# Performance work log

Hardware: AMD Instinct MI355X
Metric: run time of the kernel (lower is better)

The kernel has to match this reference:

```python
import jax, jax.numpy as jnp
import numpy as np

B, S, H = 4, 8192, 1024


def setup_inputs() -> dict:
    key = jax.random.key(0)
    kq, kk, kv, k1, k2, k3, k4 = jax.random.split(key, 7)
    residual_init_factor = 1.0
    return {
        "q": jax.random.normal(kq, (B, S, H), dtype=jnp.float32),
        "k": jax.random.normal(kk, (B, S, H), dtype=jnp.float32),
        "v": jax.random.normal(kv, (B, S, H), dtype=jnp.float32),
        "w_q": 0.01 * jax.random.normal(k1, (H, H), dtype=jnp.float32),
        "w_k": 0.01 * jax.random.normal(k2, (H, H), dtype=jnp.float32),
        "w_v": 0.01 * jax.random.normal(k3, (H, H), dtype=jnp.float32),
        "w_p": 0.01 * residual_init_factor * jax.random.normal(k4, (H, H), dtype=jnp.float32),
    }


def reference(q, k, v, w_q, w_k, w_v, w_p):
    # Projections: [B,S,H] @ [H,H]
    emb_q = jnp.einsum("bsh,hd->bsd", q, w_q)
    emb_k = jnp.einsum("bsh,hd->bsd", k, w_k)
    emb_v = jnp.einsum("bsh,hd->bsd", v, w_v)
    # AFT-simple: per-channel exponential-weighted causal prefix average
    k_exp = jnp.exp(emb_k)
    k_exp_prefix = jnp.cumsum(k_exp, axis=1)
    k_exp_v_prefix = jnp.cumsum(k_exp * emb_v, axis=1)
    y = jax.nn.sigmoid(emb_q) * (k_exp_v_prefix / k_exp_prefix)
    return jnp.einsum("bsh,hd->bsd", y, w_p)
```

## Files before the change

kernel.cpp:

```cpp
#include <hip/hip_runtime.h>
#include <hip/hip_bf16.h>
#include <cstdint>

#define AS_GLOBAL __attribute__((address_space(1)))
#define AS_LDS    __attribute__((address_space(3)))

typedef __attribute__((ext_vector_type(8))) short bf16x8;
typedef __attribute__((ext_vector_type(4))) float f32x4;

static __device__ __forceinline__ ushort f2bf(float x) {
    union { float f; uint32_t u; } c;
    c.f = x;
    uint32_t u = c.u;
    u += 0x7fffu + ((u >> 16) & 1u);
    return (ushort)(u >> 16);
}
static __device__ __forceinline__ float bf2f(ushort u) {
    union { uint32_t i; float f; } c;
    c.i = ((uint32_t)u) << 16;
    return c.f;
}

static __device__ __forceinline__ void gload_lds16(const void* g, void* l) {
    __builtin_amdgcn_global_load_lds(
        (const AS_GLOBAL uint32_t*)(uintptr_t)g,
        (AS_LDS uint32_t*)(uint32_t)(uintptr_t)l,
        16, 0, 0);
}

__global__ __launch_bounds__(256)
void transpose_to_bf16(const float* __restrict__ w, ushort* __restrict__ wt, int K, int N) {
    __shared__ float tile[32][33];
    int bn = blockIdx.x * 32;
    int bk = blockIdx.y * 32;
    int tx = threadIdx.x & 31, ty = threadIdx.x >> 5;
    #pragma unroll
    for (int i = 0; i < 32; i += 8)
        tile[ty + i][tx] = w[(size_t)(bk + ty + i) * N + bn + tx];
    __syncthreads();
    #pragma unroll
    for (int i = 0; i < 32; i += 8)
        wt[(size_t)(bn + ty + i) * K + bk + tx] = f2bf(tile[tx][ty + i]);
}

template<int EPI, int A_F32, int OUT_BF>
__global__ __launch_bounds__(512, 2)
void gemm256(const void* __restrict__ Av, const ushort* __restrict__ Bt,
             void* __restrict__ Cv) {
    constexpr int K = 1024, N = 1024;
    __shared__ ushort sA[2][16384];
    __shared__ ushort sB[2][16384];
    const int tid  = threadIdx.x;
    const int wid  = tid >> 6;
    const int lane = tid & 63;
    const int wr = wid >> 2, wc = wid & 3;
    const int lr = lane & 15, kb = lane >> 4;

    const int wg = blockIdx.x;
    const int xcd = wg & 7, local = wg >> 3;
    const int bm = xcd * 16 + (local >> 2);
    const int bn = local & 3;
    const int m0 = bm * 256, n0 = bn * 256;

    const float*  Af = (const float*)Av;
    const ushort* Ab = (const ushort*)Av;

    f32x4 acc[8][4] = {};
    float4 fa0, fa1, fa2, fa3;
    const int arl  = tid >> 2;
    const int aseg = tid & 3;
    const int agr0 = ((arl >> 6) << 7) + (arl & 63);

    auto stageB = [&](int tile, int h) {
        ushort* buf = sB[tile & 1];
        const int kt0 = tile * 64;
        #pragma unroll
        for (int j = 0; j < 2; j++) {
            const int row0 = j * 128 + h * 32 + (wid >> 2) * 64 + (wid & 3) * 8;
            const int row  = row0 + (lane >> 3);
            const int kslot = (lane & 7) ^ (lane >> 3);
            gload_lds16(Bt + (size_t)(n0 + row) * K + kt0 + kslot * 8,
                        &buf[row * 64 + (lane & 7) * 8]);
        }
    };
    auto stageAbf = [&](int tile, int h) {
        ushort* buf = sA[tile & 1];
        const int kt0 = tile * 64;
        #pragma unroll
        for (int j = 0; j < 2; j++) {
            const int row0 = j * 128 + h * 64 + wid * 8;
            const int row  = row0 + (lane >> 3);
            const int kslot = (lane & 7) ^ (lane >> 3);
            gload_lds16(Ab + (size_t)(m0 + row) * K + kt0 + kslot * 8,
                        &buf[row * 64 + (lane & 7) * 8]);
        }
    };
    auto issueA = [&](int tile, int h) {
        const int row = agr0 + h * 64;
        const float* s = Af + (size_t)(m0 + row) * K + tile * 64 + aseg * 16;
        fa0 = *(const float4*)(s);     fa1 = *(const float4*)(s + 4);
        fa2 = *(const float4*)(s + 8); fa3 = *(const float4*)(s + 12);
    };
    auto writeAcore = [&](int tile, int h) {
        const int row = agr0 + h * 64;
        const int ks0 = (aseg * 2) ^ (row & 7);
        ushort* buf = sA[tile & 1];
        bf16x8 lo, hi;
        lo[0]=(short)f2bf(fa0.x); lo[1]=(short)f2bf(fa0.y); lo[2]=(short)f2bf(fa0.z); lo[3]=(short)f2bf(fa0.w);
        lo[4]=(short)f2bf(fa1.x); lo[5]=(short)f2bf(fa1.y); lo[6]=(short)f2bf(fa1.z); lo[7]=(short)f2bf(fa1.w);
        hi[0]=(short)f2bf(fa2.x); hi[1]=(short)f2bf(fa2.y); hi[2]=(short)f2bf(fa2.z); hi[3]=(short)f2bf(fa2.w);
        hi[4]=(short)f2bf(fa3.x); hi[5]=(short)f2bf(fa3.y); hi[6]=(short)f2bf(fa3.z); hi[7]=(short)f2bf(fa3.w);
        *(bf16x8*)&buf[row * 64 + ks0 * 8]       = lo;
        *(bf16x8*)&buf[row * 64 + (ks0 ^ 1) * 8] = hi;
    };
    auto writeA = [&](int tile, int h) {
        asm volatile("s_waitcnt vmcnt(2)" ::: "memory");
        writeAcore(tile, h);
        asm volatile("s_waitcnt lgkmcnt(0)" ::: "memory");
    };

    if (A_F32) {
        #pragma unroll
        for (int x = 0; x < 2; x++)
            #pragma unroll
            for (int h = 0; h < 2; h++) {
                issueA(x, h);
                asm volatile("s_waitcnt vmcnt(0)" ::: "memory");
                writeAcore(x, h);
            }
    } else {
        #pragma unroll
        for (int x = 0; x < 2; x++) { stageAbf(x, 0); stageAbf(x, 1); }
    }
    #pragma unroll
    for (int x = 0; x < 2; x++) { stageB(x, 0); stageB(x, 1); }
    asm volatile("s_waitcnt vmcnt(0)" ::: "memory");
    __syncthreads();

#define PHASE(TOFF, MQ, NQ, STAGE_BLOCK) { \
    const ushort* pA = sA[(t0 + TOFF) & 1]; \
    const ushort* pB = sB[(t0 + TOFF) & 1]; \
    bf16x8 af[4][2], bv[2][2]; \
    _Pragma("unroll") for (int m = 0; m < 4; m++) \
      _Pragma("unroll") for (int kh = 0; kh < 2; kh++) \
        af[m][kh] = *(const bf16x8*)&pA[(wr*128 + MQ*64 + m*16 + lr)*64 + (((kh*4+kb) ^ (lr&7)))*8]; \
    _Pragma("unroll") for (int n = 0; n < 2; n++) \
      _Pragma("unroll") for (int kh = 0; kh < 2; kh++) \
        bv[n][kh] = *(const bf16x8*)&pB[(wc*64 + NQ*32 + n*16 + lr)*64 + (((kh*4+kb) ^ (lr&7)))*8]; \
    STAGE_BLOCK \
    asm volatile("s_waitcnt vmcnt(6)" ::: "memory"); \
    asm volatile("" ::: "memory"); \
    __builtin_amdgcn_s_barrier(); \
    asm volatile("" ::: "memory"); \
    __builtin_amdgcn_s_setprio(1); \
    _Pragma("unroll") for (int m = 0; m < 4; m++) \
      _Pragma("unroll") for (int n = 0; n < 2; n++) { \
        acc[MQ*4+m][NQ*2+n] = __builtin_amdgcn_mfma_f32_16x16x32_bf16(af[m][0], bv[n][0], acc[MQ*4+m][NQ*2+n], 0, 0, 0); \
        acc[MQ*4+m][NQ*2+n] = __builtin_amdgcn_mfma_f32_16x16x32_bf16(af[m][1], bv[n][1], acc[MQ*4+m][NQ*2+n], 0, 0, 0); \
      } \
    __builtin_amdgcn_s_setprio(0); \
    asm volatile("" ::: "memory"); \
    __builtin_amdgcn_s_barrier(); \
    asm volatile("" ::: "memory"); \
}

    for (int i = 0; i < 8; i++) {
        const int t0 = 2 * i;
        PHASE(0, 0, 0, {
            if (i > 0) {
                if (A_F32) writeA(t0 + 1, 0); 
                if (A_F32) issueA(t0 + 1, 1); else stageAbf(t0 + 1, 1);
            }
        })
        PHASE(0, 0, 1, { if (i > 0) stageB(t0 + 1, 1); })
        PHASE(0, 1, 0, {
            if (A_F32 && i > 0) writeA(t0 + 1, 1);
            if (i < 7) { if (A_F32) issueA(t0 + 2, 0); else stageAbf(t0 + 2, 0); }
        })
        PHASE(0, 1, 1, {
            if (i < 7) stageB(t0 + 2, 0);
            if (i == 7) asm volatile("s_waitcnt vmcnt(0)" ::: "memory");
        })
        PHASE(1, 0, 0, {
            if (i < 7) {
                if (A_F32) writeA(t0 + 2, 0);
                if (A_F32) issueA(t0 + 2, 1); else stageAbf(t0 + 2, 1);
            }
        })
        PHASE(1, 0, 1, { if (i < 7) stageB(t0 + 2, 1); })
        PHASE(1, 1, 0, {
            if (i < 7) {
                if (A_F32) writeA(t0 + 2, 1);
                if (A_F32) issueA(t0 + 3, 0); else stageAbf(t0 + 3, 0);
            }
        })
        PHASE(1, 1, 1, { if (i < 7) stageB(t0 + 3, 0); })
    }
#undef PHASE

    float*  Cf = (float*)Cv;
    ushort* Cb = (ushort*)Cv;
    #pragma unroll
    for (int fm = 0; fm < 8; fm++) {
        #pragma unroll
        for (int fn = 0; fn < 4; fn++) {
            #pragma unroll
            for (int r = 0; r < 4; r++) {
                int row = m0 + wr * 128 + fm * 16 + (lane >> 4) * 4 + r;
                int col = n0 + wc * 64 + fn * 16 + lr;
                float v = acc[fm][fn][r];
                if (EPI == 1) v = 1.0f / (1.0f + __expf(-v));
                else if (EPI == 2) v = __expf(v);
                size_t idx = (size_t)row * N + col;
                if (OUT_BF) Cb[idx] = f2bf(v);
                else        Cf[idx] = v;
            }
        }
    }
}

__global__ __launch_bounds__(256)
void scan_partials(const ushort* __restrict__ ke, const ushort* __restrict__ ev,
                   float* __restrict__ pke, float* __restrict__ pkv) {
    const int H = 1024, S = 8192, CHUNK = 32, BH = 4096;
    int h0 = threadIdx.x * 4;
    int c = blockIdx.x;
    int b = blockIdx.y;
    size_t base = ((size_t)b * S + (size_t)c * CHUNK) * H + h0;
    float se0 = 0.f, se1 = 0.f, se2 = 0.f, se3 = 0.f;
    float sv0 = 0.f, sv1 = 0.f, sv2 = 0.f, sv3 = 0.f;
    for (int s = 0; s < CHUNK; s++) {
        ushort4 e4 = *(const ushort4*)(ke + base + (size_t)s * H);
        ushort4 v4 = *(const ushort4*)(ev + base + (size_t)s * H);
        float e0 = bf2f(e4.x), e1 = bf2f(e4.y), e2 = bf2f(e4.z), e3 = bf2f(e4.w);
        se0 += e0; se1 += e1; se2 += e2; se3 += e3;
        sv0 += e0 * bf2f(v4.x); sv1 += e1 * bf2f(v4.y);
        sv2 += e2 * bf2f(v4.z); sv3 += e3 * bf2f(v4.w);
    }
    size_t p = (size_t)c * BH + b * H + h0;
    *(float4*)(pke + p) = make_float4(se0, se1, se2, se3);
    *(float4*)(pkv + p) = make_float4(sv0, sv1, sv2, sv3);
}

__global__ __launch_bounds__(256)
void scan_offsets(float* __restrict__ pke, float* __restrict__ pkv, int nch, int BH) {
    int i = blockIdx.x * blockDim.x + threadIdx.x;
    if (i >= BH) return;
    float rke = 0.f, rkv = 0.f;
    for (int c = 0; c < nch; c++) {
        size_t idx = (size_t)c * BH + i;
        float a = pke[idx], b = pkv[idx];
        pke[idx] = rke; pkv[idx] = rkv;
        rke += a; rkv += b;
    }
}

__global__ __launch_bounds__(256)
void scan_final(const ushort* __restrict__ ke, const ushort* __restrict__ ev,
                const ushort* __restrict__ sq,
                const float* __restrict__ pke, const float* __restrict__ pkv,
                ushort* __restrict__ ybf) {
    const int H = 1024, S = 8192, CHUNK = 32, BH = 4096;
    int h0 = threadIdx.x * 4;
    int c = blockIdx.x;
    int b = blockIdx.y;
    size_t p = (size_t)c * BH + b * H + h0;
    float4 rke = *(const float4*)(pke + p);
    float4 rkv = *(const float4*)(pkv + p);
    size_t base = ((size_t)b * S + (size_t)c * CHUNK) * H + h0;
    for (int s = 0; s < CHUNK; s++) {
        size_t idx = base + (size_t)s * H;
        ushort4 e4 = *(const ushort4*)(ke + idx);
        ushort4 v4 = *(const ushort4*)(ev + idx);
        ushort4 q4 = *(const ushort4*)(sq + idx);
        float e0 = bf2f(e4.x), e1 = bf2f(e4.y), e2 = bf2f(e4.z), e3 = bf2f(e4.w);
        rke.x += e0; rke.y += e1; rke.z += e2; rke.w += e3;
        rkv.x += e0 * bf2f(v4.x); rkv.y += e1 * bf2f(v4.y);
        rkv.z += e2 * bf2f(v4.z); rkv.w += e3 * bf2f(v4.w);
        ushort4 o;
        o.x = f2bf(bf2f(q4.x) * (rkv.x / rke.x));
        o.y = f2bf(bf2f(q4.y) * (rkv.y / rke.y));
        o.z = f2bf(bf2f(q4.z) * (rkv.z / rke.z));
        o.w = f2bf(bf2f(q4.w) * (rkv.w / rke.w));
        *(ushort4*)(ybf + idx) = o;
    }
}

extern "C" void kernel_launch(void* const* d_in, const int* in_sizes, int n_in,
                              void* d_out, int out_size, void* d_ws, size_t ws_size,
                              hipStream_t stream) {
    const float* q   = (const float*)d_in[0];
    const float* k   = (const float*)d_in[1];
    const float* v   = (const float*)d_in[2];
    const float* w_q = (const float*)d_in[3];
    const float* w_k = (const float*)d_in[4];
    const float* w_v = (const float*)d_in[5];
    const float* w_p = (const float*)d_in[6];
    float* out = (float*)d_out;

    const int B = 4, S = 8192, H = 1024;
    const int M = B * S;
    const size_t MH = (size_t)M * H;
    const int NCH = 256;
    const int BH = B * H;

    char* ws = (char*)d_ws;
    size_t off = 0;
    auto alloc = [&](size_t bytes) -> char* {
        char* p = ws + off;
        off += (bytes + 255) & ~(size_t)255;
        return p;
    };
    ushort* ybuf = (ushort*)alloc(MH * 2);
    ushort* wqt  = (ushort*)alloc((size_t)H * H * 2);
    ushort* wkt  = (ushort*)alloc((size_t)H * H * 2);
    ushort* wvt  = (ushort*)alloc((size_t)H * H * 2);
    ushort* wpt  = (ushort*)alloc((size_t)H * H * 2);
    ushort* sqb  = (ushort*)alloc(MH * 2);
    ushort* keb  = (ushort*)alloc(MH * 2);
    ushort* evb  = (ushort*)alloc(MH * 2);
    float*  pke  = (float*)alloc((size_t)NCH * BH * 4);
    float*  pkv  = (float*)alloc((size_t)NCH * BH * 4);

    dim3 tg(H / 32, H / 32);
    const int ngg = (M / 256) * (H / 256);
    dim3 gs(NCH, B);

    transpose_to_bf16<<<tg, 256, 0, stream>>>(w_q, wqt, H, H);
    transpose_to_bf16<<<tg, 256, 0, stream>>>(w_k, wkt, H, H);
    transpose_to_bf16<<<tg, 256, 0, stream>>>(w_v, wvt, H, H);
    transpose_to_bf16<<<tg, 256, 0, stream>>>(w_p, wpt, H, H);

    gemm256<1, 1, 1><<<ngg, 512, 0, stream>>>(q, wqt, sqb);
    gemm256<2, 1, 1><<<ngg, 512, 0, stream>>>(k, wkt, keb);
    gemm256<0, 1, 1><<<ngg, 512, 0, stream>>>(v, wvt, evb);

    scan_partials<<<gs, 256, 0, stream>>>(keb, evb, pke, pkv);
    scan_offsets<<<BH / 256, 256, 0, stream>>>(pke, pkv, NCH, BH);
    scan_final<<<gs, 256, 0, stream>>>(keb, evb, sqb, pke, pkv, ybuf);

    gemm256<0, 0, 0><<<ngg, 512, 0, stream>>>(ybuf, wpt, out);
}
```

Baseline: 550.1 us.

## Double-buffer MFMA operand fragments in registers across GEMM phases

Adds two register sets for the A and B fragments (X/Y) and loads the next phase's operands from LDS before the current phase's MFMAs. The old scheme read and consumed them inside the same phase. The quadrant order changes to (0,0),(1,0),(0,1),(1,1) so fragments can be reused across phases, and the next tile's first fragments are prefetched during the last phase. The aim is to hide LDS read latency behind matrix-core work. The cost is roughly 96 extra VGPRs, which could cut occupancy or cause spills. Some reads now sit before a phase's barrier, so the visibility of the staged data depends on earlier waits.

```diff
diff --git a/kernel.cpp b/kernel.cpp
--- a/kernel.cpp
+++ b/kernel.cpp
@@ -66,6 +66,8 @@
     const ushort* Ab = (const ushort*)Av;
 
     f32x4 acc[8][4] = {};
+    bf16x8 afX[4][2], afY[4][2];
+    bf16x8 bvX[2][2], bvY[2][2];
     float4 fa0, fa1, fa2, fa3;
     const int arl  = tid >> 2;
     const int aseg = tid & 3;
@@ -119,6 +121,32 @@
         asm volatile("s_waitcnt lgkmcnt(0)" ::: "memory");
     };
 
+    auto readAF = [&](bf16x8 (&dst)[4][2], int tile, int MQ) {
+        const ushort* pA = sA[tile & 1];
+        #pragma unroll
+        for (int m = 0; m < 4; m++)
+            #pragma unroll
+            for (int kh = 0; kh < 2; kh++)
+                dst[m][kh] = *(const bf16x8*)&pA[(wr*128 + MQ*64 + m*16 + lr)*64 + (((kh*4+kb) ^ (lr&7)))*8];
+    };
+    auto readBV = [&](bf16x8 (&dst)[2][2], int tile, int NQ) {
+        const ushort* pB = sB[tile & 1];
+        #pragma unroll
+        for (int n = 0; n < 2; n++)
+            #pragma unroll
+            for (int kh = 0; kh < 2; kh++)
+                dst[n][kh] = *(const bf16x8*)&pB[(wc*64 + NQ*32 + n*16 + lr)*64 + (((kh*4+kb) ^ (lr&7)))*8];
+    };
+    auto mfma16 = [&](bf16x8 (&AF)[4][2], bf16x8 (&BV)[2][2], int MQ, int NQ) {
+        #pragma unroll
+        for (int m = 0; m < 4; m++)
+            #pragma unroll
+            for (int n = 0; n < 2; n++) {
+                acc[MQ*4+m][NQ*2+n] = __builtin_amdgcn_mfma_f32_16x16x32_bf16(AF[m][0], BV[n][0], acc[MQ*4+m][NQ*2+n], 0, 0, 0);
+                acc[MQ*4+m][NQ*2+n] = __builtin_amdgcn_mfma_f32_16x16x32_bf16(AF[m][1], BV[n][1], acc[MQ*4+m][NQ*2+n], 0, 0, 0);
+            }
+    };
+
     if (A_F32) {
         #pragma unroll
         for (int x = 0; x < 2; x++)
@@ -136,28 +164,17 @@
     for (int x = 0; x < 2; x++) { stageB(x, 0); stageB(x, 1); }
     asm volatile("s_waitcnt vmcnt(0)" ::: "memory");
     __syncthreads();
-
-#define PHASE(TOFF, MQ, NQ, STAGE_BLOCK) { \
-    const ushort* pA = sA[(t0 + TOFF) & 1]; \
-    const ushort* pB = sB[(t0 + TOFF) & 1]; \
-    bf16x8 af[4][2], bv[2][2]; \
-    _Pragma("unroll") for (int m = 0; m < 4; m++) \
-      _Pragma("unroll") for (int kh = 0; kh < 2; kh++) \
-        af[m][kh] = *(const bf16x8*)&pA[(wr*128 + MQ*64 + m*16 + lr)*64 + (((kh*4+kb) ^ (lr&7)))*8]; \
-    _Pragma("unroll") for (int n = 0; n < 2; n++) \
-      _Pragma("unroll") for (int kh = 0; kh < 2; kh++) \
-        bv[n][kh] = *(const bf16x8*)&pB[(wc*64 + NQ*32 + n*16 + lr)*64 + (((kh*4+kb) ^ (lr&7)))*8]; \
-    STAGE_BLOCK \
+    readAF(afX, 0, 0);
+    readBV(bvX, 0, 0);
+
+#define PHASE(AF, BV, MQ, NQ, READS, STAGES) { \
+    READS \
+    STAGES \
     asm volatile("s_waitcnt vmcnt(6)" ::: "memory"); \
-    asm volatile("" ::: "memory"); \
     __builtin_amdgcn_s_barrier(); \
     asm volatile("" ::: "memory"); \
     __builtin_amdgcn_s_setprio(1); \
-    _Pragma("unroll") for (int m = 0; m < 4; m++) \
-      _Pragma("unroll") for (int n = 0; n < 2; n++) { \
-        acc[MQ*4+m][NQ*2+n] = __builtin_amdgcn_mfma_f32_16x16x32_bf16(af[m][0], bv[n][0], acc[MQ*4+m][NQ*2+n], 0, 0, 0); \
-        acc[MQ*4+m][NQ*2+n] = __builtin_amdgcn_mfma_f32_16x16x32_bf16(af[m][1], bv[n][1], acc[MQ*4+m][NQ*2+n], 0, 0, 0); \
-      } \
+    mfma16(AF, BV, MQ, NQ); \
     __builtin_amdgcn_s_setprio(0); \
     asm volatile("" ::: "memory"); \
     __builtin_amdgcn_s_barrier(); \
@@ -166,35 +183,41 @@
 
     for (int i = 0; i < 8; i++) {
         const int t0 = 2 * i;
-        PHASE(0, 0, 0, {
-            if (i > 0) {
-                if (A_F32) writeA(t0 + 1, 0); 
-                if (A_F32) issueA(t0 + 1, 1); else stageAbf(t0 + 1, 1);
-            }
-        })
-        PHASE(0, 0, 1, { if (i > 0) stageB(t0 + 1, 1); })
-        PHASE(0, 1, 0, {
-            if (A_F32 && i > 0) writeA(t0 + 1, 1);
-            if (i < 7) { if (A_F32) issueA(t0 + 2, 0); else stageAbf(t0 + 2, 0); }
-        })
-        PHASE(0, 1, 1, {
-            if (i < 7) stageB(t0 + 2, 0);
-            if (i == 7) asm volatile("s_waitcnt vmcnt(0)" ::: "memory");
-        })
-        PHASE(1, 0, 0, {
-            if (i < 7) {
-                if (A_F32) writeA(t0 + 2, 0);
-                if (A_F32) issueA(t0 + 2, 1); else stageAbf(t0 + 2, 1);
-            }
-        })
-        PHASE(1, 0, 1, { if (i < 7) stageB(t0 + 2, 1); })
-        PHASE(1, 1, 0, {
-            if (i < 7) {
-                if (A_F32) writeA(t0 + 2, 1);
-                if (A_F32) issueA(t0 + 3, 0); else stageAbf(t0 + 3, 0);
-            }
-        })
-        PHASE(1, 1, 1, { if (i < 7) stageB(t0 + 3, 0); })
+        PHASE(afX, bvX, 0, 0,
+            { readAF(afY, t0, 1); },
+            { if (i > 0) {
+                  if (A_F32) { writeA(t0 + 1, 0); issueA(t0 + 1, 1); }
+                  else stageAbf(t0 + 1, 1);
+              } })
+        PHASE(afY, bvX, 1, 0,
+            { readBV(bvY, t0, 1); },
+            { if (i > 0) stageB(t0 + 1, 1); })
+        PHASE(afX, bvY, 0, 1,
+            { },
+            { if (A_F32 && i > 0) writeA(t0 + 1, 1);
+              if (i < 7) { if (A_F32) issueA(t0 + 2, 0); else stageAbf(t0 + 2, 0); } })
+        PHASE(afY, bvY, 1, 1,
+            { readAF(afX, t0 + 1, 0); readBV(bvX, t0 + 1, 0); },
+            { if (i < 7) stageB(t0 + 2, 0);
+              if (i == 7) asm volatile("s_waitcnt vmcnt(0)" ::: "memory"); })
+        PHASE(afX, bvX, 0, 0,
+            { readAF(afY, t0 + 1, 1); },
+            { if (i < 7) {
+                  if (A_F32) { writeA(t0 + 2, 0); issueA(t0 + 2, 1); }
+                  else stageAbf(t0 + 2, 1);
+              } })
+        PHASE(afY, bvX, 1, 0,
+            { readBV(bvY, t0 + 1, 1); },
+            { if (i < 7) stageB(t0 + 2, 1); })
+        PHASE(afX, bvY, 0, 1,
+            { },
+            { if (i < 7) {
+                  if (A_F32) { writeA(t0 + 2, 1); issueA(t0 + 3, 0); }
+                  else stageAbf(t0 + 3, 0);
+              } })
+        PHASE(afY, bvY, 1, 1,
+            { if (i < 7) { readAF(afX, t0 + 2, 0); readBV(bvX, t0 + 2, 0); } },
+            { if (i < 7) stageB(t0 + 3, 0); })
     }
 #undef PHASE
 
```

Result: slower. 968.7 us (+76.1%).
